# Kernel tuning notes

Measured on AMD Instinct MI355X. Metric: run time of the kernel, lower is better.

Reference implementation:

```python
import jax, jax.numpy as jnp
import numpy as np

N_NODES = 100000
N_EDGES = 3200000
NODE_DIM = 16      # output_size_node
EDGE_IN = 2 * NODE_DIM  # input_size_Edge = 32
EDGE_OUT = 9
HIDDEN = 9
MSG_ROUNDS = 3


def _mlp_params(key, d_in, d_hid, d_out):
    k1, k2, k3 = jax.random.split(key, 3)
    s1 = 1.0 / np.sqrt(d_in)
    s2 = 1.0 / np.sqrt(d_hid)
    return (
        jax.random.normal(k1, (d_in, d_hid), jnp.float32) * s1,
        jnp.zeros((d_hid,), jnp.float32),
        jax.random.normal(k2, (d_hid, d_hid), jnp.float32) * s2,
        jnp.zeros((d_hid,), jnp.float32),
        jax.random.normal(k3, (d_hid, d_out), jnp.float32) * s2,
        jnp.zeros((d_out,), jnp.float32),
    )


def setup_inputs() -> dict:
    key = jax.random.key(0)
    kx, ks, kd, kfe, kfx = jax.random.split(key, 5)
    X = jax.random.normal(kx, (N_NODES, NODE_DIM), jnp.float32)
    edge_src = jax.random.randint(ks, (N_EDGES,), 0, N_NODES, jnp.int32)
    edge_dst = jax.random.randint(kd, (N_EDGES,), 0, N_NODES, jnp.int32)
    fe = _mlp_params(kfe, EDGE_IN, HIDDEN, EDGE_OUT)
    fx = _mlp_params(kfx, EDGE_OUT + NODE_DIM, HIDDEN, NODE_DIM)
    return {
        "X": X, "edge_src": edge_src, "edge_dst": edge_dst,
        "fe_W1": fe[0], "fe_b1": fe[1], "fe_W2": fe[2], "fe_b2": fe[3], "fe_W3": fe[4], "fe_b3": fe[5],
        "fx_W1": fx[0], "fx_b1": fx[1], "fx_W2": fx[2], "fx_b2": fx[3], "fx_W3": fx[4], "fx_b3": fx[5],
    }


def _mlp3(h, W1, b1, W2, b2, W3, b3):
    # 3-layer MLP with relu hidden activations (MLP_nonlinear, act='relu')
    h = jax.nn.relu(h @ W1 + b1)
    h = jax.nn.relu(h @ W2 + b2)
    return h @ W3 + b3


def reference(X, edge_src, edge_dst,
              fe_W1, fe_b1, fe_W2, fe_b2, fe_W3, fe_b3,
              fx_W1, fx_b1, fx_W2, fx_b2, fx_W3, fx_b3):
    n = X.shape[0]
    for _ in range(MSG_ROUNDS):
        # per-edge message: fe(cat(X[i], X[j])) with i=receiver(dst), j=sender(src)
        e_in = jnp.concatenate([X[edge_dst], X[edge_src]], axis=-1)  # [E, 2*D]
        msgs = _mlp3(e_in, fe_W1, fe_b1, fe_W2, fe_b2, fe_W3, fe_b3)  # [E, 9]
        m = jax.ops.segment_sum(msgs, edge_dst, num_segments=n)       # [N, 9]
        # per-node update: fx(cat(X[i], m_i))
        X = _mlp3(jnp.concatenate([X, m], axis=-1),
                  fx_W1, fx_b1, fx_W2, fx_b2, fx_W3, fx_b3)           # [N, D]
    return X
```

## Files before the change

kernel.cpp:

```cpp
#include <hip/hip_runtime.h>


constexpr int NN = 100000;
constexpr int NE = 3200000;
constexpr int NB_CNT = (NN + 255) / 256;


__global__ __launch_bounds__(256) void hist_k(const int* __restrict__ dst,
                                              int* __restrict__ cnt,
                                              unsigned short* __restrict__ rank)
{
    int e = blockIdx.x * 256 + threadIdx.x;
    if (e >= NE) return;
    int d = dst[e];
    rank[e] = (unsigned short)atomicAdd(&cnt[d], 1);
}

__global__ __launch_bounds__(256) void blocksum_k(const int* __restrict__ cnt,
                                                  int* __restrict__ bsum)
{
    __shared__ int red[256];
    int t = threadIdx.x;
    int i = blockIdx.x * 256 + t;
    red[t] = (i < NN) ? cnt[i] : 0;
    __syncthreads();
    for (int off = 128; off > 0; off >>= 1) {
        if (t < off) red[t] += red[t + off];
        __syncthreads();
    }
    if (t == 0) bsum[blockIdx.x] = red[0];
}

__global__ __launch_bounds__(512) void scanpart_k(const int* __restrict__ bsum,
                                                  int* __restrict__ boff, int nb)
{
    __shared__ int s[512];
    int t = threadIdx.x;
    int v = (t < nb) ? bsum[t] : 0;
    s[t] = v;
    __syncthreads();
    for (int off = 1; off < 512; off <<= 1) {
        int a = (t >= off) ? s[t - off] : 0;
        __syncthreads();
        s[t] += a;
        __syncthreads();
    }
    if (t < nb) boff[t] = s[t] - v;
}

__global__ __launch_bounds__(256) void rowstart_k(const int* __restrict__ cnt,
                                                  const int* __restrict__ boff,
                                                  int* __restrict__ row_start)
{
    __shared__ int s[256];
    int t = threadIdx.x;
    int i = blockIdx.x * 256 + t;
    int v = (i < NN) ? cnt[i] : 0;
    s[t] = v;
    __syncthreads();
    for (int off = 1; off < 256; off <<= 1) {
        int a = (t >= off) ? s[t - off] : 0;
        __syncthreads();
        s[t] += a;
        __syncthreads();
    }
    int incl = s[t];
    if (i < NN) row_start[i] = boff[blockIdx.x] + incl - v;
    if (i == NN - 1) row_start[NN] = boff[blockIdx.x] + incl;
}

__global__ __launch_bounds__(256) void scatter_k(const int* __restrict__ src,
                                                 const int* __restrict__ dst,
                                                 const unsigned short* __restrict__ rank,
                                                 const int* __restrict__ row_start,
                                                 unsigned long long* __restrict__ sed)
{
    int e = blockIdx.x * 256 + threadIdx.x;
    if (e >= NE) return;
    int d = dst[e];
    int pos = row_start[d] + (int)rank[e];
    sed[pos] = ((unsigned long long)(unsigned)d << 32) | (unsigned)src[e];
}


__global__ __launch_bounds__(256) void base_k(const float* __restrict__ X,
                                              const float* __restrict__ feW1,
                                              const float* __restrict__ feb1,
                                              float* __restrict__ base1,
                                              float* __restrict__ bases,
                                              float* __restrict__ m)
{
    __shared__ float sW[32 * 12], sb[9];
    const int t = threadIdx.x;
    for (int i = t; i < 288; i += 256) sW[(i / 9) * 12 + (i % 9)] = feW1[i];
    if (t < 9) sb[t] = feb1[t];
    __syncthreads();

    const int n = blockIdx.x * 256 + t;
    if (n >= NN) return;

    float x[16];
    const float4* p = reinterpret_cast<const float4*>(X + (size_t)n * 16);
    #pragma unroll
    for (int q = 0; q < 4; ++q) {
        float4 v = p[q];
        x[4*q] = v.x; x[4*q+1] = v.y; x[4*q+2] = v.z; x[4*q+3] = v.w;
    }
    float bd[9];
    #pragma unroll
    for (int j = 0; j < 9; ++j) bd[j] = sb[j];
    #pragma unroll
    for (int i = 0; i < 16; ++i) {
        const float xi = x[i];
        #pragma unroll
        for (int j = 0; j < 9; ++j) bd[j] = fmaf(xi, sW[i * 12 + j], bd[j]);
    }
    float bs[9];
    #pragma unroll
    for (int j = 0; j < 9; ++j) bs[j] = 0.f;
    #pragma unroll
    for (int i = 0; i < 16; ++i) {
        const float xi = x[i];
        #pragma unroll
        for (int j = 0; j < 9; ++j) bs[j] = fmaf(xi, sW[(16 + i) * 12 + j], bs[j]);
    }
    float* bp = base1 + (size_t)n * 12;
    #pragma unroll
    for (int j = 0; j < 9; ++j) bp[j] = bd[j];
    float* sp = bases + (size_t)n * 16;
    #pragma unroll
    for (int j = 0; j < 9; ++j) sp[j] = bs[j];
    float* mp = m + (size_t)n * 9;
    #pragma unroll
    for (int j = 0; j < 9; ++j) mp[j] = 0.f;
}


__global__ __launch_bounds__(256) void edge2_k(
    const float* __restrict__ base1,
    const float* __restrict__ bases,
    const unsigned long long* __restrict__ sed,
    const float* __restrict__ feW2, const float* __restrict__ feb2,
    const float* __restrict__ feW3, const float* __restrict__ feb3,
    float* __restrict__ m)
{
    __shared__ float sW2[9 * 12], sW3[9 * 12], sb2[9], sb3[9];
    const int t = threadIdx.x;
    if (t < 81)  sW2[(t / 9) * 12 + (t % 9)] = feW2[t];
    if (t >= 128 && t < 209) { int i = t - 128; sW3[(i / 9) * 12 + (i % 9)] = feW3[i]; }
    if (t >= 224 && t < 233) sb2[t - 224] = feb2[t - 224];
    if (t >= 240 && t < 249) sb3[t - 240] = feb3[t - 240];
    __syncthreads();

    const int e = blockIdx.x * 256 + t;
    const unsigned long long pk = sed[e];
    const int d = (int)(pk >> 32);
    const int s = (int)(pk & 0xffffffffu);

    float a[9];
    {
        const float4* pb = reinterpret_cast<const float4*>(base1 + (size_t)d * 12);
        float4 b0 = pb[0], b1 = pb[1];
        const float4* ps = reinterpret_cast<const float4*>(bases + (size_t)s * 16);
        float4 c0 = ps[0], c1 = ps[1];
        a[0] = b0.x + c0.x; a[1] = b0.y + c0.y; a[2] = b0.z + c0.z; a[3] = b0.w + c0.w;
        a[4] = b1.x + c1.x; a[5] = b1.y + c1.y; a[6] = b1.z + c1.z; a[7] = b1.w + c1.w;
        a[8] = base1[(size_t)d * 12 + 8] + bases[(size_t)s * 16 + 8];
    }
    #pragma unroll
    for (int j = 0; j < 9; ++j) a[j] = fmaxf(a[j], 0.f);

    float h2[9];
    #pragma unroll
    for (int j = 0; j < 9; ++j) h2[j] = sb2[j];
    #pragma unroll
    for (int i = 0; i < 9; ++i) {
        const float ai = a[i];
        #pragma unroll
        for (int j = 0; j < 9; ++j) h2[j] = fmaf(ai, sW2[i * 12 + j], h2[j]);
    }
    #pragma unroll
    for (int j = 0; j < 9; ++j) h2[j] = fmaxf(h2[j], 0.f);

    float o[9];
    #pragma unroll
    for (int j = 0; j < 9; ++j) o[j] = sb3[j];
    #pragma unroll
    for (int i = 0; i < 9; ++i) {
        const float hi = h2[i];
        #pragma unroll
        for (int j = 0; j < 9; ++j) o[j] = fmaf(hi, sW3[i * 12 + j], o[j]);
    }

    const int lane = t & 63;
    const int dprev = __shfl_up(d, 1);
    const bool head = (lane == 0) || (dprev != d);
    const unsigned long long hm = __ballot(head);
    const int dist = __clzll((long long)(hm << (63 - lane)));
    #pragma unroll
    for (int off = 1; off < 64; off <<= 1) {
        const bool ok = (dist >= off);
        #pragma unroll
        for (int j = 0; j < 9; ++j) {
            const float ov = __shfl_up(o[j], off);
            o[j] += ok ? ov : 0.f;
        }
    }
    const bool tail = (lane == 63) || (((hm >> (lane + 1)) & 1ull) != 0ull);
    if (tail) {
        float* mp = m + (size_t)d * 9;
        #pragma unroll
        for (int j = 0; j < 9; ++j) atomicAdd(mp + j, o[j]);
    }
}


__global__ __launch_bounds__(256) void node2_k(
    const float* __restrict__ Xin, float* __restrict__ m,
    const float* __restrict__ fxW1, const float* __restrict__ fxb1,
    const float* __restrict__ fxW2, const float* __restrict__ fxb2,
    const float* __restrict__ fxW3, const float* __restrict__ fxb3,
    const float* __restrict__ feW1, const float* __restrict__ feb1,
    float* __restrict__ Xout, float* __restrict__ base1out,
    float* __restrict__ basesout)
{
    __shared__ float sU1[25 * 12], sU2[9 * 12], sU3[9 * 16];
    __shared__ float sW1d[16 * 12], sW1s[16 * 12];
    __shared__ float sNB[34], sEB1[9];
    const int t = threadIdx.x;
    if (t < 225) sU1[(t / 9) * 12 + (t % 9)] = fxW1[t];
    if (t < 81)  sU2[(t / 9) * 12 + (t % 9)] = fxW2[t];
    if (t < 144) sU3[t] = fxW3[t];
    if (t < 144) sW1d[(t / 9) * 12 + (t % 9)] = feW1[t];
    if (t >= 112) { int i = t - 112; sW1s[(i / 9) * 12 + (i % 9)] = feW1[144 + i]; }
    if (t < 9) sNB[t] = fxb1[t];
    if (t >= 32 && t < 41) sNB[9 + (t - 32)] = fxb2[t - 32];
    if (t >= 64 && t < 80) sNB[18 + (t - 64)] = fxb3[t - 64];
    if (t >= 96 && t < 105) sEB1[t - 96] = feb1[t - 96];
    __syncthreads();

    const int n = blockIdx.x * 256 + t;
    if (n >= NN) return;

    float xr[16];
    {
        const float4* p = reinterpret_cast<const float4*>(Xin + (size_t)n * 16);
        #pragma unroll
        for (int q = 0; q < 4; ++q) {
            float4 v = p[q];
            xr[4*q] = v.x; xr[4*q+1] = v.y; xr[4*q+2] = v.z; xr[4*q+3] = v.w;
        }
    }
    float mm[9];
    float* mp = m + (size_t)n * 9;
    #pragma unroll
    for (int j = 0; j < 9; ++j) mm[j] = mp[j];
    #pragma unroll
    for (int j = 0; j < 9; ++j) mp[j] = 0.f;

    float h1[9];
    #pragma unroll
    for (int j = 0; j < 9; ++j) h1[j] = sNB[j];
    #pragma unroll
    for (int i = 0; i < 16; ++i) {
        const float xi = xr[i];
        #pragma unroll
        for (int j = 0; j < 9; ++j) h1[j] = fmaf(xi, sU1[i * 12 + j], h1[j]);
    }
    #pragma unroll
    for (int i = 0; i < 9; ++i) {
        const float xi = mm[i];
        #pragma unroll
        for (int j = 0; j < 9; ++j) h1[j] = fmaf(xi, sU1[(16 + i) * 12 + j], h1[j]);
    }
    #pragma unroll
    for (int j = 0; j < 9; ++j) h1[j] = fmaxf(h1[j], 0.f);

    float h2[9];
    #pragma unroll
    for (int j = 0; j < 9; ++j) h2[j] = sNB[9 + j];
    #pragma unroll
    for (int i = 0; i < 9; ++i) {
        const float xi = h1[i];
        #pragma unroll
        for (int j = 0; j < 9; ++j) h2[j] = fmaf(xi, sU2[i * 12 + j], h2[j]);
    }
    #pragma unroll
    for (int j = 0; j < 9; ++j) h2[j] = fmaxf(h2[j], 0.f);

    float o[16];
    #pragma unroll
    for (int k = 0; k < 16; ++k) o[k] = sNB[18 + k];
    #pragma unroll
    for (int j = 0; j < 9; ++j) {
        const float hj = h2[j];
        #pragma unroll
        for (int k = 0; k < 16; ++k) o[k] = fmaf(hj, sU3[j * 16 + k], o[k]);
    }

    float4* po = reinterpret_cast<float4*>(Xout + (size_t)n * 16);
    #pragma unroll
    for (int q = 0; q < 4; ++q) {
        float4 v;
        v.x = o[4*q]; v.y = o[4*q+1]; v.z = o[4*q+2]; v.w = o[4*q+3];
        po[q] = v;
    }

    float b[9];
    #pragma unroll
    for (int j = 0; j < 9; ++j) b[j] = sEB1[j];
    #pragma unroll
    for (int i = 0; i < 16; ++i) {
        const float xi = o[i];
        #pragma unroll
        for (int j = 0; j < 9; ++j) b[j] = fmaf(xi, sW1d[i * 12 + j], b[j]);
    }
    float* bp = base1out + (size_t)n * 12;
    #pragma unroll
    for (int j = 0; j < 9; ++j) bp[j] = b[j];

    float c[9];
    #pragma unroll
    for (int j = 0; j < 9; ++j) c[j] = 0.f;
    #pragma unroll
    for (int i = 0; i < 16; ++i) {
        const float xi = o[i];
        #pragma unroll
        for (int j = 0; j < 9; ++j) c[j] = fmaf(xi, sW1s[i * 12 + j], c[j]);
    }
    float* sp = basesout + (size_t)n * 16;
    #pragma unroll
    for (int j = 0; j < 9; ++j) sp[j] = c[j];
}

extern "C" void kernel_launch(void* const* d_in, const int* in_sizes, int n_in,
                              void* d_out, int out_size, void* d_ws, size_t ws_size,
                              hipStream_t stream)
{
    const float* X0   = (const float*)d_in[0];
    const int*   esrc = (const int*)d_in[1];
    const int*   edst = (const int*)d_in[2];
    const float* feW1 = (const float*)d_in[3];
    const float* feb1 = (const float*)d_in[4];
    const float* feW2 = (const float*)d_in[5];
    const float* feb2 = (const float*)d_in[6];
    const float* feW3 = (const float*)d_in[7];
    const float* feb3 = (const float*)d_in[8];
    const float* fxW1 = (const float*)d_in[9];
    const float* fxb1 = (const float*)d_in[10];
    const float* fxW2 = (const float*)d_in[11];
    const float* fxb2 = (const float*)d_in[12];
    const float* fxW3 = (const float*)d_in[13];
    const float* fxb3 = (const float*)d_in[14];
    float* out = (float*)d_out;

    float* Xa        = (float*)d_ws;
    int*   cnt       = (int*)(Xa + (size_t)NN * 16);
    int*   row_start = cnt + NN;
    int*   bsum      = row_start + (NN + 2);
    int*   boff      = bsum + (NB_CNT + 1);
    float* base1     = (float*)(boff + (NB_CNT + 1));
    float* mb        = base1 + (size_t)NN * 12;
    float* base_s    = mb + (size_t)NN * 9;
    unsigned short* rank = (unsigned short*)base1;
    unsigned long long* sed =
        (unsigned long long*)(base_s + (size_t)NN * 16);

    const dim3 thr(256);
    const dim3 gE(NE / 256);
    const dim3 gN(NB_CNT);

    hipMemsetAsync(cnt, 0, (size_t)NN * sizeof(int), stream);
    hist_k<<<gE, thr, 0, stream>>>(edst, cnt, rank);
    blocksum_k<<<gN, thr, 0, stream>>>(cnt, bsum);
    scanpart_k<<<1, 512, 0, stream>>>(bsum, boff, NB_CNT);
    rowstart_k<<<gN, thr, 0, stream>>>(cnt, boff, row_start);
    scatter_k<<<gE, thr, 0, stream>>>(esrc, edst, rank, row_start, sed);

    base_k<<<gN, thr, 0, stream>>>(X0, feW1, feb1, base1, base_s, mb);
    edge2_k<<<gE, thr, 0, stream>>>(base1, base_s, sed, feW2, feb2, feW3, feb3, mb);
    node2_k<<<gN, thr, 0, stream>>>(X0, mb, fxW1, fxb1, fxW2, fxb2, fxW3, fxb3,
                                    feW1, feb1, Xa, base1, base_s);
    edge2_k<<<gE, thr, 0, stream>>>(base1, base_s, sed, feW2, feb2, feW3, feb3, mb);
    node2_k<<<gN, thr, 0, stream>>>(Xa, mb, fxW1, fxb1, fxW2, fxb2, fxW3, fxb3,
                                    feW1, feb1, out, base1, base_s);
    edge2_k<<<gE, thr, 0, stream>>>(base1, base_s, sed, feW2, feb2, feW3, feb3, mb);
    node2_k<<<gN, thr, 0, stream>>>(out, mb, fxW1, fxb1, fxW2, fxb2, fxW3, fxb3,
                                    feW1, feb1, Xa, base1, base_s);

    hipMemcpyAsync(out, Xa, (size_t)NN * 16 * sizeof(float),
                   hipMemcpyDeviceToDevice, stream);
}
```

Baseline: 560.4 us.

## Replace full CSR sort with bucketed partial sort and LDS segment sums

Replaces the per-destination counting sort (histogram, scans, scatter) with a single-pass block-local bucketing of edges into fixed-capacity slots of 128 destination nodes, packed as 32-bit words. The edge kernel now processes one bucket per block, keeps destination bases in LDS and accumulates messages with LDS atomics before a single coalesced write of m, replacing wave-level segmented scans and global atomics. It also drops m zeroing and the final device copy. The fixed SLOT capacity of 8192 edges per bucket assumes a bounded in-degree distribution, and bucket-order is nondeterministic, so float summation order varies between runs.

After: 801.5 us. 1.43x slower.

```diff
diff --git a/kernel.cpp b/kernel.cpp
--- a/kernel.cpp
+++ b/kernel.cpp
@@ -3,83 +3,63 @@
 
 constexpr int NN = 100000;
 constexpr int NE = 3200000;
-constexpr int NB_CNT = (NN + 255) / 256;
-
-
-__global__ __launch_bounds__(256) void hist_k(const int* __restrict__ dst,
-                                              int* __restrict__ cnt,
-                                              unsigned short* __restrict__ rank)
-{
-    int e = blockIdx.x * 256 + threadIdx.x;
-    if (e >= NE) return;
-    int d = dst[e];
-    rank[e] = (unsigned short)atomicAdd(&cnt[d], 1);
-}
-
-__global__ __launch_bounds__(256) void blocksum_k(const int* __restrict__ cnt,
-                                                  int* __restrict__ bsum)
-{
-    __shared__ int red[256];
-    int t = threadIdx.x;
-    int i = blockIdx.x * 256 + t;
-    red[t] = (i < NN) ? cnt[i] : 0;
-    __syncthreads();
-    for (int off = 128; off > 0; off >>= 1) {
-        if (t < off) red[t] += red[t + off];
-        __syncthreads();
-    }
-    if (t == 0) bsum[blockIdx.x] = red[0];
-}
-
-__global__ __launch_bounds__(512) void scanpart_k(const int* __restrict__ bsum,
-                                                  int* __restrict__ boff, int nb)
-{
-    __shared__ int s[512];
-    int t = threadIdx.x;
-    int v = (t < nb) ? bsum[t] : 0;
-    s[t] = v;
-    __syncthreads();
-    for (int off = 1; off < 512; off <<= 1) {
-        int a = (t >= off) ? s[t - off] : 0;
-        __syncthreads();
-        s[t] += a;
-        __syncthreads();
-    }
-    if (t < nb) boff[t] = s[t] - v;
-}
-
-__global__ __launch_bounds__(256) void rowstart_k(const int* __restrict__ cnt,
-                                                  const int* __restrict__ boff,
-                                                  int* __restrict__ row_start)
-{
-    __shared__ int s[256];
-    int t = threadIdx.x;
-    int i = blockIdx.x * 256 + t;
-    int v = (i < NN) ? cnt[i] : 0;
-    s[t] = v;
-    __syncthreads();
-    for (int off = 1; off < 256; off <<= 1) {
-        int a = (t >= off) ? s[t - off] : 0;
-        __syncthreads();
-        s[t] += a;
-        __syncthreads();
-    }
-    int incl = s[t];
-    if (i < NN) row_start[i] = boff[blockIdx.x] + incl - v;
-    if (i == NN - 1) row_start[NN] = boff[blockIdx.x] + incl;
-}
-
-__global__ __launch_bounds__(256) void scatter_k(const int* __restrict__ src,
-                                                 const int* __restrict__ dst,
-                                                 const unsigned short* __restrict__ rank,
-                                                 const int* __restrict__ row_start,
-                                                 unsigned long long* __restrict__ sed)
-{
-    int e = blockIdx.x * 256 + threadIdx.x;
-    if (e >= NE) return;
-    int d = dst[e];
-    int pos = row_start[d] + (int)rank[e];
-    sed[pos] = ((unsigned long long)(unsigned)d << 32) | (unsigned)src[e];
+constexpr int NBK = (NN + 127) / 128;
+constexpr int SLOT = 8192;
+constexpr int EPB = 4096;
+constexpr int NBLK_SORT = (NE + EPB - 1) / EPB;
+constexpr int NB_NODE = (NN + 255) / 256;
+
+
+__global__ __launch_bounds__(256) void init_k(int* __restrict__ gcursor)
+{
+    int i = blockIdx.x * 256 + threadIdx.x;
+    if (i < NBK) gcursor[i] = i * SLOT;
+}
+
+
+__global__ __launch_bounds__(256) void bsort_k(const int* __restrict__ src,
+                                               const int* __restrict__ dst,
+                                               int* __restrict__ gcursor,
+                                               unsigned* __restrict__ sed)
+{
+    __shared__ int lhist[NBK];
+    __shared__ int lbase[NBK];
+    const int t = threadIdx.x;
+    for (int i = t; i < NBK; i += 256) lhist[i] = 0;
+    __syncthreads();
+
+    const int blkbase = blockIdx.x * EPB;
+    unsigned pr[16], sv[16];
+    #pragma unroll
+    for (int k = 0; k < 16; ++k) {
+        const int e = blkbase + k * 256 + t;
+        if (e < NE) {
+            const int d = dst[e];
+            const int s = src[e];
+            const int bin = d >> 7;
+            const int r = atomicAdd(&lhist[bin], 1);
+            pr[k] = ((unsigned)bin << 13) | (unsigned)r;
+            sv[k] = ((unsigned)(d & 127) << 17) | (unsigned)s;
+        } else {
+            pr[k] = 0xFFFFFFFFu;
+        }
+    }
+    __syncthreads();
+
+    for (int i = t; i < NBK; i += 256) {
+        const int c = lhist[i];
+        if (c) lbase[i] = atomicAdd(&gcursor[i], c);
+    }
+    __syncthreads();
+
+    #pragma unroll
+    for (int k = 0; k < 16; ++k) {
+        if (pr[k] != 0xFFFFFFFFu) {
+            const int bin = (int)(pr[k] >> 13);
+            const int r = (int)(pr[k] & 0x1FFFu);
+            sed[lbase[bin] + r] = sv[k];
+        }
+    }
 }
 
 
@@ -87,8 +67,7 @@
                                               const float* __restrict__ feW1,
                                               const float* __restrict__ feb1,
                                               float* __restrict__ base1,
-                                              float* __restrict__ bases,
-                                              float* __restrict__ m)
+                                              float* __restrict__ bases)
 {
     __shared__ float sW[32 * 12], sb[9];
     const int t = threadIdx.x;
@@ -124,99 +103,97 @@
         #pragma unroll
         for (int j = 0; j < 9; ++j) bs[j] = fmaf(xi, sW[(16 + i) * 12 + j], bs[j]);
     }
-    float* bp = base1 + (size_t)n * 12;
+    float* bp = base1 + (size_t)n * 9;
     #pragma unroll
     for (int j = 0; j < 9; ++j) bp[j] = bd[j];
     float* sp = bases + (size_t)n * 16;
     #pragma unroll
     for (int j = 0; j < 9; ++j) sp[j] = bs[j];
-    float* mp = m + (size_t)n * 9;
-    #pragma unroll
-    for (int j = 0; j < 9; ++j) mp[j] = 0.f;
-}
-
-
-__global__ __launch_bounds__(256) void edge2_k(
+}
+
+
+__global__ __launch_bounds__(512) void edge3_k(
     const float* __restrict__ base1,
     const float* __restrict__ bases,
-    const unsigned long long* __restrict__ sed,
+    const unsigned* __restrict__ sed,
+    const int* __restrict__ gcursor,
     const float* __restrict__ feW2, const float* __restrict__ feb2,
     const float* __restrict__ feW3, const float* __restrict__ feb3,
     float* __restrict__ m)
 {
     __shared__ float sW2[9 * 12], sW3[9 * 12], sb2[9], sb3[9];
+    __shared__ float b1l[128 * 12];
+    __shared__ float ml[128 * 9];
     const int t = threadIdx.x;
+    const int b = blockIdx.x;
+
     if (t < 81)  sW2[(t / 9) * 12 + (t % 9)] = feW2[t];
     if (t >= 128 && t < 209) { int i = t - 128; sW3[(i / 9) * 12 + (i % 9)] = feW3[i]; }
     if (t >= 224 && t < 233) sb2[t - 224] = feb2[t - 224];
     if (t >= 240 && t < 249) sb3[t - 240] = feb3[t - 240];
-    __syncthreads();
-
-    const int e = blockIdx.x * 256 + t;
-    const unsigned long long pk = sed[e];
-    const int d = (int)(pk >> 32);
-    const int s = (int)(pk & 0xffffffffu);
-
-    float a[9];
-    {
-        const float4* pb = reinterpret_cast<const float4*>(base1 + (size_t)d * 12);
-        float4 b0 = pb[0], b1 = pb[1];
-        const float4* ps = reinterpret_cast<const float4*>(bases + (size_t)s * 16);
-        float4 c0 = ps[0], c1 = ps[1];
-        a[0] = b0.x + c0.x; a[1] = b0.y + c0.y; a[2] = b0.z + c0.z; a[3] = b0.w + c0.w;
-        a[4] = b1.x + c1.x; a[5] = b1.y + c1.y; a[6] = b1.z + c1.z; a[7] = b1.w + c1.w;
-        a[8] = base1[(size_t)d * 12 + 8] + bases[(size_t)s * 16 + 8];
-    }
-    #pragma unroll
-    for (int j = 0; j < 9; ++j) a[j] = fmaxf(a[j], 0.f);
-
-    float h2[9];
-    #pragma unroll
-    for (int j = 0; j < 9; ++j) h2[j] = sb2[j];
-    #pragma unroll
-    for (int i = 0; i < 9; ++i) {
-        const float ai = a[i];
-        #pragma unroll
-        for (int j = 0; j < 9; ++j) h2[j] = fmaf(ai, sW2[i * 12 + j], h2[j]);
-    }
-    #pragma unroll
-    for (int j = 0; j < 9; ++j) h2[j] = fmaxf(h2[j], 0.f);
-
-    float o[9];
-    #pragma unroll
-    for (int j = 0; j < 9; ++j) o[j] = sb3[j];
-    #pragma unroll
-    for (int i = 0; i < 9; ++i) {
-        const float hi = h2[i];
-        #pragma unroll
-        for (int j = 0; j < 9; ++j) o[j] = fmaf(hi, sW3[i * 12 + j], o[j]);
-    }
-
-    const int lane = t & 63;
-    const int dprev = __shfl_up(d, 1);
-    const bool head = (lane == 0) || (dprev != d);
-    const unsigned long long hm = __ballot(head);
-    const int dist = __clzll((long long)(hm << (63 - lane)));
-    #pragma unroll
-    for (int off = 1; off < 64; off <<= 1) {
-        const bool ok = (dist >= off);
-        #pragma unroll
-        for (int j = 0; j < 9; ++j) {
-            const float ov = __shfl_up(o[j], off);
-            o[j] += ok ? ov : 0.f;
-        }
-    }
-    const bool tail = (lane == 63) || (((hm >> (lane + 1)) & 1ull) != 0ull);
-    if (tail) {
-        float* mp = m + (size_t)d * 9;
-        #pragma unroll
-        for (int j = 0; j < 9; ++j) atomicAdd(mp + j, o[j]);
-    }
+
+    const int nbase = b * 128;
+    const int nn = (NN - nbase < 128) ? (NN - nbase) : 128;
+    for (int i = t; i < nn * 9; i += 512)
+        b1l[(i / 9) * 12 + (i % 9)] = base1[(size_t)nbase * 9 + i];
+    for (int i = t; i < 128 * 9; i += 512) ml[i] = 0.f;
+    __syncthreads();
+
+    const int eend = gcursor[b];
+    for (int e = b * SLOT + t; e < eend; e += 512) {
+        const unsigned pk = sed[e];
+        const int s = (int)(pk & 0x1FFFFu);
+        const int dl = (int)(pk >> 17);
+
+        float a[9];
+        {
+            const float4* ps = reinterpret_cast<const float4*>(bases + (size_t)s * 16);
+            float4 c0 = ps[0], c1 = ps[1];
+            const float c8 = bases[(size_t)s * 16 + 8];
+            const float4* pb = reinterpret_cast<const float4*>(&b1l[dl * 12]);
+            float4 b0 = pb[0], b1 = pb[1];
+            const float b8 = b1l[dl * 12 + 8];
+            a[0] = b0.x + c0.x; a[1] = b0.y + c0.y; a[2] = b0.z + c0.z; a[3] = b0.w + c0.w;
+            a[4] = b1.x + c1.x; a[5] = b1.y + c1.y; a[6] = b1.z + c1.z; a[7] = b1.w + c1.w;
+            a[8] = b8 + c8;
+        }
+        #pragma unroll
+        for (int j = 0; j < 9; ++j) a[j] = fmaxf(a[j], 0.f);
+
+        float h2[9];
+        #pragma unroll
+        for (int j = 0; j < 9; ++j) h2[j] = sb2[j];
+        #pragma unroll
+        for (int i = 0; i < 9; ++i) {
+            const float ai = a[i];
+            #pragma unroll
+            for (int j = 0; j < 9; ++j) h2[j] = fmaf(ai, sW2[i * 12 + j], h2[j]);
+        }
+        #pragma unroll
+        for (int j = 0; j < 9; ++j) h2[j] = fmaxf(h2[j], 0.f);
+
+        float o[9];
+        #pragma unroll
+        for (int j = 0; j < 9; ++j) o[j] = sb3[j];
+        #pragma unroll
+        for (int i = 0; i < 9; ++i) {
+            const float hi = h2[i];
+            #pragma unroll
+            for (int j = 0; j < 9; ++j) o[j] = fmaf(hi, sW3[i * 12 + j], o[j]);
+        }
+
+        const int d9 = dl * 9;
+        #pragma unroll
+        for (int j = 0; j < 9; ++j) atomicAdd(&ml[d9 + j], o[j]);
+    }
+    __syncthreads();
+
+    for (int i = t; i < nn * 9; i += 512) m[(size_t)nbase * 9 + i] = ml[i];
 }
 
 
 __global__ __launch_bounds__(256) void node2_k(
-    const float* __restrict__ Xin, float* __restrict__ m,
+    const float* __restrict__ Xin, const float* __restrict__ m,
     const float* __restrict__ fxW1, const float* __restrict__ fxb1,
     const float* __restrict__ fxW2, const float* __restrict__ fxb2,
     const float* __restrict__ fxW3, const float* __restrict__ fxb3,
@@ -252,11 +229,9 @@
         }
     }
     float mm[9];
-    float* mp = m + (size_t)n * 9;
+    const float* mp = m + (size_t)n * 9;
     #pragma unroll
     for (int j = 0; j < 9; ++j) mm[j] = mp[j];
-    #pragma unroll
-    for (int j = 0; j < 9; ++j) mp[j] = 0.f;
 
     float h1[9];
     #pragma unroll
@@ -306,37 +281,38 @@
         po[q] = v;
     }
 
-    float b[9];
-    #pragma unroll
-    for (int j = 0; j < 9; ++j) b[j] = sEB1[j];
+    float bb[9];
+    #pragma unroll
+    for (int j = 0; j < 9; ++j) bb[j] = sEB1[j];
     #pragma unroll
     for (int i = 0; i < 16; ++i) {
         const float xi = o[i];
         #pragma unroll
-        for (int j = 0; j < 9; ++j) b[j] = fmaf(xi, sW1d[i * 12 + j], b[j]);
-    }
-    float* bp = base1out + (size_t)n * 12;
-    #pragma unroll
-    for (int j = 0; j < 9; ++j) bp[j] = b[j];
-
-    float c[9];
-    #pragma unroll
-    for (int j = 0; j < 9; ++j) c[j] = 0.f;
+        for (int j = 0; j < 9; ++j) bb[j] = fmaf(xi, sW1d[i * 12 + j], bb[j]);
+    }
+    float* bp = base1out + (size_t)n * 9;
+    #pragma unroll
+    for (int j = 0; j < 9; ++j) bp[j] = bb[j];
+
+    float cc[9];
+    #pragma unroll
+    for (int j = 0; j < 9; ++j) cc[j] = 0.f;
     #pragma unroll
     for (int i = 0; i < 16; ++i) {
         const float xi = o[i];
         #pragma unroll
-        for (int j = 0; j < 9; ++j) c[j] = fmaf(xi, sW1s[i * 12 + j], c[j]);
+        for (int j = 0; j < 9; ++j) cc[j] = fmaf(xi, sW1s[i * 12 + j], cc[j]);
     }
     float* sp = basesout + (size_t)n * 16;
     #pragma unroll
-    for (int j = 0; j < 9; ++j) sp[j] = c[j];
+    for (int j = 0; j < 9; ++j) sp[j] = cc[j];
 }
 
 extern "C" void kernel_launch(void* const* d_in, const int* in_sizes, int n_in,
                               void* d_out, int out_size, void* d_ws, size_t ws_size,
                               hipStream_t stream)
 {
+    (void)in_sizes; (void)n_in; (void)out_size; (void)ws_size;
     const float* X0   = (const float*)d_in[0];
     const int*   esrc = (const int*)d_in[1];
     const int*   edst = (const int*)d_in[2];
@@ -354,40 +330,32 @@
     const float* fxb3 = (const float*)d_in[14];
     float* out = (float*)d_out;
 
-    float* Xa        = (float*)d_ws;
-    int*   cnt       = (int*)(Xa + (size_t)NN * 16);
-    int*   row_start = cnt + NN;
-    int*   bsum      = row_start + (NN + 2);
-    int*   boff      = bsum + (NB_CNT + 1);
-    float* base1     = (float*)(boff + (NB_CNT + 1));
-    float* mb        = base1 + (size_t)NN * 12;
-    float* base_s    = mb + (size_t)NN * 9;
-    unsigned short* rank = (unsigned short*)base1;
-    unsigned long long* sed =
-        (unsigned long long*)(base_s + (size_t)NN * 16);
+    float* Xa     = (float*)d_ws;
+    float* base1  = Xa + (size_t)NN * 16;
+    float* bases  = base1 + (size_t)NN * 9;
+    float* mb     = bases + (size_t)NN * 16;
+    int* gcursor  = (int*)(mb + (size_t)NN * 9);
+    unsigned* sed = (unsigned*)(gcursor + 1024);
 
     const dim3 thr(256);
-    const dim3 gE(NE / 256);
-    const dim3 gN(NB_CNT);
-
-    hipMemsetAsync(cnt, 0, (size_t)NN * sizeof(int), stream);
-    hist_k<<<gE, thr, 0, stream>>>(edst, cnt, rank);
-    blocksum_k<<<gN, thr, 0, stream>>>(cnt, bsum);
-    scanpart_k<<<1, 512, 0, stream>>>(bsum, boff, NB_CNT);
-    rowstart_k<<<gN, thr, 0, stream>>>(cnt, boff, row_start);
-    scatter_k<<<gE, thr, 0, stream>>>(esrc, edst, rank, row_start, sed);
-
-    base_k<<<gN, thr, 0, stream>>>(X0, feW1, feb1, base1, base_s, mb);
-    edge2_k<<<gE, thr, 0, stream>>>(base1, base_s, sed, feW2, feb2, feW3, feb3, mb);
+    const dim3 gS(NBLK_SORT);
+    const dim3 gB(NBK);
+    const dim3 gN(NB_NODE);
+
+    init_k<<<4, thr, 0, stream>>>(gcursor);
+    bsort_k<<<gS, thr, 0, stream>>>(esrc, edst, gcursor, sed);
+
+    base_k<<<gN, thr, 0, stream>>>(X0, feW1, feb1, base1, bases);
+    edge3_k<<<gB, dim3(512), 0, stream>>>(base1, bases, sed, gcursor,
+                                          feW2, feb2, feW3, feb3, mb);
     node2_k<<<gN, thr, 0, stream>>>(X0, mb, fxW1, fxb1, fxW2, fxb2, fxW3, fxb3,
-                                    feW1, feb1, Xa, base1, base_s);
-    edge2_k<<<gE, thr, 0, stream>>>(base1, base_s, sed, feW2, feb2, feW3, feb3, mb);
+                                    feW1, feb1, Xa, base1, bases);
+    edge3_k<<<gB, dim3(512), 0, stream>>>(base1, bases, sed, gcursor,
+                                          feW2, feb2, feW3, feb3, mb);
     node2_k<<<gN, thr, 0, stream>>>(Xa, mb, fxW1, fxb1, fxW2, fxb2, fxW3, fxb3,
-                                    feW1, feb1, out, base1, base_s);
-    edge2_k<<<gE, thr, 0, stream>>>(base1, base_s, sed, feW2, feb2, feW3, feb3, mb);
+                                    feW1, feb1, out, base1, bases);
+    edge3_k<<<gB, dim3(512), 0, stream>>>(base1, bases, sed, gcursor,
+                                          feW2, feb2, feW3, feb3, mb);
     node2_k<<<gN, thr, 0, stream>>>(out, mb, fxW1, fxb1, fxW2, fxb2, fxW3, fxb3,
-                                    feW1, feb1, Xa, base1, base_s);
-
-    hipMemcpyAsync(out, Xa, (size_t)NN * 16 * sizeof(float),
-                   hipMemcpyDeviceToDevice, stream);
-}
+                                    feW1, feb1, out, base1, bases);
+}
```
